# Kernel optimization log

Measured on AMD Instinct MI355X. Metric: run time of the kernel, lower is better.

Reference implementation:

```python
import jax, jax.numpy as jnp
import numpy as np

B, S, D_IN, D_OUT = 4, 2048, 4096, 11008


def setup_inputs() -> dict:
    key = jax.random.key(0)
    kx, kw, ks, kb = jax.random.split(key, 4)
    x = jax.random.normal(kx, (B, S, D_IN), dtype=jnp.float32)
    # Simulate fp8 storage: values are exactly representable in float8_e4m3fn.
    w_raw = jax.random.normal(kw, (D_OUT, D_IN), dtype=jnp.float32)
    w_q = w_raw.astype(jnp.float8_e4m3fn).astype(jnp.float32)
    # Per-output-channel dequant scale (positive).
    scale = jax.random.uniform(ks, (D_OUT, 1), dtype=jnp.float32, minval=0.01, maxval=0.1)
    bias = jax.random.normal(kb, (D_OUT,), dtype=jnp.float32)
    return {"x": x, "w_q": w_q, "scale": scale, "bias": bias}


def reference(x, w_q, scale, bias):
    # dequantize_tensor: fp8 payload * per-channel scale -> full-precision weight [D_OUT, D_IN]
    w = w_q * scale
    # F.linear(x, w, bias) = x @ w.T + bias
    out = jnp.einsum('bsd,od->bso', x, w) + bias
    return out
```

## Files before the change

kernel.cpp:

```cpp
#include <hip/hip_runtime.h>
#include <hip/hip_bf16.h>
#include <stdint.h>

#define M_DIM 8192
#define N_DIM 11008
#define K_DIM 4096
#define BM 256
#define BN 256
#define BK 32
#define NT (K_DIM / BK)
#define NBX (N_DIM / BN)
#define NBY (M_DIM / BM)
#define NBLK (NBX * NBY)
#define CPX (NBLK / 8)

typedef __bf16 bf16_8 __attribute__((ext_vector_type(8)));
typedef float f32x4 __attribute__((ext_vector_type(4)));

__device__ __forceinline__ uint32_t pack_bf2(float lo, float hi) {
    uint32_t ulo = __float_as_uint(lo);
    uint32_t uhi = __float_as_uint(hi);
    ulo = (ulo + 0x7fffu + ((ulo >> 16) & 1u)) >> 16;
    uhi = (uhi + 0x7fffu + ((uhi >> 16) & 1u)) >> 16;
    return ulo | (uhi << 16);
}

__global__ __launch_bounds__(256) void cvt_f32_bf16(const float* __restrict__ src,
                                                    uint2* __restrict__ dst, int n4) {
    int i = blockIdx.x * 256 + threadIdx.x;
    if (i >= n4) return;
    float4 a = ((const float4*)src)[i];
    uint2 o;
    o.x = pack_bf2(a.x, a.y);
    o.y = pack_bf2(a.z, a.w);
    dst[i] = o;
}

__device__ __forceinline__ void load_lds16(const __bf16* g, __bf16* l) {
    __builtin_amdgcn_global_load_lds(
        (__attribute__((address_space(1))) void*)(g),
        (__attribute__((address_space(3))) void*)(l),
        16, 0, 0);
}

#define VMCNT(n) asm volatile("s_waitcnt vmcnt(" #n ")" ::: "memory")
#define CFENCE asm volatile("" ::: "memory")

__device__ __forceinline__ void wg_barrier() {
    CFENCE;
    __builtin_amdgcn_s_barrier();
    CFENCE;
}

__device__ __forceinline__ void stage_tile(const __bf16* Ag, const __bf16* Wg,
                                           __bf16* Asl, __bf16* Bsl,
                                           int wave, long ko) {
    __bf16* la = Asl + wave * 16 * BK;
    __bf16* lb = Bsl + wave * 16 * BK;
    load_lds16(Ag + ko, la);
    load_lds16(Ag + 128 * (long)K_DIM + ko, la + 128 * BK);
    load_lds16(Wg + ko, lb);
    load_lds16(Wg + 128 * (long)K_DIM + ko, lb + 128 * BK);
}

__device__ __forceinline__ void compute_step(const __bf16* __restrict__ Abase,
                                             const __bf16* __restrict__ Bbase,
                                             f32x4 (&acc)[8][4]) {
    bf16_8 af[8], bv[4];
#pragma unroll
    for (int i = 0; i < 8; i++) af[i] = *(const bf16_8*)(Abase + i * 16 * BK);
#pragma unroll
    for (int j = 0; j < 4; j++) bv[j] = *(const bf16_8*)(Bbase + j * 16 * BK);
    __builtin_amdgcn_s_setprio(1);
#pragma unroll
    for (int i = 0; i < 8; i++)
#pragma unroll
        for (int j = 0; j < 4; j++)
            acc[i][j] = __builtin_amdgcn_mfma_f32_16x16x32_bf16(af[i], bv[j], acc[i][j], 0, 0, 0);
    __builtin_amdgcn_s_setprio(0);
}

__global__ __launch_bounds__(512, 2) void gemm_bt_scaled(
    const __bf16* __restrict__ A, const __bf16* __restrict__ W,
    const float* __restrict__ scale, const float* __restrict__ bias,
    float* __restrict__ C) {
    __shared__ __align__(16) __bf16 As[4][BM * BK];
    __shared__ __align__(16) __bf16 Bs[4][BN * BK];

    const int t = threadIdx.x;
    const int wave = t >> 6;
    const int lane = t & 63;
    const int wm = wave >> 2;
    const int wn = wave & 3;

    const int bid = (int)blockIdx.x;
    const int swz = (bid & 7) * CPX + (bid >> 3);
    const int by = swz / NBX;
    const int bx = swz - by * NBX;
    const int m0 = by * BM;
    const int n0 = bx * BN;

    const int srow = lane >> 2;
    const int sch = ((lane & 3) ^ ((lane >> 3) & 3)) * 8;
    const __bf16* Ag = A + (long)(m0 + wave * 16 + srow) * K_DIM + sch;
    const __bf16* Wg = W + (long)(n0 + wave * 16 + srow) * K_DIM + sch;

    const int lrow = lane & 15;
    const int swzr = (lrow >> 1) & 3;
    const int lk = ((lane >> 4) ^ swzr) * 8;
    const int aoff = (wm * 128 + lrow) * BK + lk;
    const int boff = (wn * 64 + lrow) * BK + lk;

    f32x4 acc[8][4] = {};

    stage_tile(Ag, Wg, &As[0][0], &Bs[0][0], wave, 0);
    stage_tile(Ag, Wg, &As[1][0], &Bs[1][0], wave, (long)BK);
    stage_tile(Ag, Wg, &As[2][0], &Bs[2][0], wave, 2L * BK);
    VMCNT(8);
    wg_barrier();

    int tt = 0;
    for (; tt < NT - 3; ++tt) {
        const int sl = tt & 3;
        const int sn = (tt + 3) & 3;
        stage_tile(Ag, Wg, &As[sn][0], &Bs[sn][0], wave, (long)(tt + 3) * BK);
        compute_step(&As[sl][aoff], &Bs[sl][boff], acc);
        VMCNT(8);
        wg_barrier();
    }
    compute_step(&As[tt & 3][aoff], &Bs[tt & 3][boff], acc);
    VMCNT(4);
    wg_barrier();
    ++tt;
    compute_step(&As[tt & 3][aoff], &Bs[tt & 3][boff], acc);
    VMCNT(0);
    wg_barrier();
    ++tt;
    compute_step(&As[tt & 3][aoff], &Bs[tt & 3][boff], acc);

    const int crow4 = (lane >> 4) * 4;
    const int ccol = lane & 15;
#pragma unroll
    for (int j = 0; j < 4; j++) {
        const int n = n0 + wn * 64 + j * 16 + ccol;
        const float sc = scale[n];
        const float bi = bias[n];
#pragma unroll
        for (int i = 0; i < 8; i++) {
            const int mbase = m0 + wm * 128 + i * 16 + crow4;
#pragma unroll
            for (int r = 0; r < 4; r++) {
                C[(long)(mbase + r) * N_DIM + n] = acc[i][j][r] * sc + bi;
            }
        }
    }
}

extern "C" void kernel_launch(void* const* d_in, const int* in_sizes, int n_in,
                              void* d_out, int out_size, void* d_ws, size_t ws_size,
                              hipStream_t stream) {
    const float* x = (const float*)d_in[0];
    const float* w_q = (const float*)d_in[1];
    const float* scale = (const float*)d_in[2];
    const float* bias = (const float*)d_in[3];
    float* out = (float*)d_out;

    __bf16* x_bf = (__bf16*)d_ws;
    __bf16* w_bf = (__bf16*)((char*)d_ws + (size_t)M_DIM * K_DIM * sizeof(__bf16));

    const int n4x = (M_DIM * K_DIM) / 4;
    const int n4w = (N_DIM * K_DIM) / 4;
    cvt_f32_bf16<<<(n4x + 255) / 256, 256, 0, stream>>>(x, (uint2*)x_bf, n4x);
    cvt_f32_bf16<<<(n4w + 255) / 256, 256, 0, stream>>>(w_q, (uint2*)w_bf, n4w);

    gemm_bt_scaled<<<dim3(NBLK), 512, 0, stream>>>(x_bf, w_bf, scale, bias, out);
}
```

Baseline: 1.533 ms.

## Split each K-step into two interleaved half-phases with staggered loads and barriers

Restructures the main loop so each K-tile is processed in two halves: read half the A fragments plus B fragments, issue the A global->LDS load, barrier, run 16 MFMAs, then read the other A half, issue the W load and run the remaining 16 MFMAs. Explicit lgkmcnt waits and sched_barriers pin the instruction order so memory issue and MFMA work from different waves interleave, in a ping-pong style. The tail is rolled into a non-unrolled loop. This adds barriers per iteration, which could cost more than the overlap gains.

```diff
diff --git a/kernel.cpp b/kernel.cpp
--- a/kernel.cpp
+++ b/kernel.cpp
@@ -44,40 +44,19 @@
 }
 
 #define VMCNT(n) asm volatile("s_waitcnt vmcnt(" #n ")" ::: "memory")
-#define CFENCE asm volatile("" ::: "memory")
+#define LGKM0    asm volatile("s_waitcnt lgkmcnt(0)" ::: "memory")
+#define SCHED0   __builtin_amdgcn_sched_barrier(0)
 
 __device__ __forceinline__ void wg_barrier() {
-    CFENCE;
+    asm volatile("" ::: "memory");
     __builtin_amdgcn_s_barrier();
-    CFENCE;
-}
-
-__device__ __forceinline__ void stage_tile(const __bf16* Ag, const __bf16* Wg,
-                                           __bf16* Asl, __bf16* Bsl,
-                                           int wave, long ko) {
-    __bf16* la = Asl + wave * 16 * BK;
-    __bf16* lb = Bsl + wave * 16 * BK;
-    load_lds16(Ag + ko, la);
-    load_lds16(Ag + 128 * (long)K_DIM + ko, la + 128 * BK);
-    load_lds16(Wg + ko, lb);
-    load_lds16(Wg + 128 * (long)K_DIM + ko, lb + 128 * BK);
-}
-
-__device__ __forceinline__ void compute_step(const __bf16* __restrict__ Abase,
-                                             const __bf16* __restrict__ Bbase,
-                                             f32x4 (&acc)[8][4]) {
-    bf16_8 af[8], bv[4];
-#pragma unroll
-    for (int i = 0; i < 8; i++) af[i] = *(const bf16_8*)(Abase + i * 16 * BK);
-#pragma unroll
-    for (int j = 0; j < 4; j++) bv[j] = *(const bf16_8*)(Bbase + j * 16 * BK);
-    __builtin_amdgcn_s_setprio(1);
-#pragma unroll
-    for (int i = 0; i < 8; i++)
-#pragma unroll
-        for (int j = 0; j < 4; j++)
-            acc[i][j] = __builtin_amdgcn_mfma_f32_16x16x32_bf16(af[i], bv[j], acc[i][j], 0, 0, 0);
-    __builtin_amdgcn_s_setprio(0);
+    asm volatile("" ::: "memory");
+}
+
+__device__ __forceinline__ void stage_pair(const __bf16* G, __bf16* L, int wave, long ko) {
+    __bf16* lw = L + wave * 16 * BK;
+    load_lds16(G + ko, lw);
+    load_lds16(G + 128L * K_DIM + ko, lw + 128 * BK);
 }
 
 __global__ __launch_bounds__(512, 2) void gemm_bt_scaled(
@@ -113,9 +92,12 @@
 
     f32x4 acc[8][4] = {};
 
-    stage_tile(Ag, Wg, &As[0][0], &Bs[0][0], wave, 0);
-    stage_tile(Ag, Wg, &As[1][0], &Bs[1][0], wave, (long)BK);
-    stage_tile(Ag, Wg, &As[2][0], &Bs[2][0], wave, 2L * BK);
+    stage_pair(Ag, &As[0][0], wave, 0);
+    stage_pair(Wg, &Bs[0][0], wave, 0);
+    stage_pair(Ag, &As[1][0], wave, (long)BK);
+    stage_pair(Wg, &Bs[1][0], wave, (long)BK);
+    stage_pair(Ag, &As[2][0], wave, 2L * BK);
+    stage_pair(Wg, &Bs[2][0], wave, 2L * BK);
     VMCNT(8);
     wg_barrier();
 
@@ -123,20 +105,68 @@
     for (; tt < NT - 3; ++tt) {
         const int sl = tt & 3;
         const int sn = (tt + 3) & 3;
-        stage_tile(Ag, Wg, &As[sn][0], &Bs[sn][0], wave, (long)(tt + 3) * BK);
-        compute_step(&As[sl][aoff], &Bs[sl][boff], acc);
+        const long ko = (long)(tt + 3) * BK;
+        const __bf16* Ab = &As[sl][aoff];
+        const __bf16* Bb = &Bs[sl][boff];
+
+        bf16_8 a0[4], bv[4];
+#pragma unroll
+        for (int i = 0; i < 4; i++) a0[i] = *(const bf16_8*)(Ab + i * 16 * BK);
+#pragma unroll
+        for (int j = 0; j < 4; j++) bv[j] = *(const bf16_8*)(Bb + j * 16 * BK);
+        stage_pair(Ag, &As[sn][0], wave, ko);
+        wg_barrier();
+        LGKM0;
+        SCHED0;
+        __builtin_amdgcn_s_setprio(1);
+#pragma unroll
+        for (int i = 0; i < 4; i++)
+#pragma unroll
+            for (int j = 0; j < 4; j++)
+                acc[i][j] = __builtin_amdgcn_mfma_f32_16x16x32_bf16(a0[i], bv[j], acc[i][j], 0, 0, 0);
+        __builtin_amdgcn_s_setprio(0);
+        SCHED0;
+        wg_barrier();
+
+        bf16_8 a1[4];
+#pragma unroll
+        for (int i = 0; i < 4; i++) a1[i] = *(const bf16_8*)(Ab + (4 + i) * 16 * BK);
+        stage_pair(Wg, &Bs[sn][0], wave, ko);
+        wg_barrier();
+        LGKM0;
+        SCHED0;
+        __builtin_amdgcn_s_setprio(1);
+#pragma unroll
+        for (int i = 0; i < 4; i++)
+#pragma unroll
+            for (int j = 0; j < 4; j++)
+                acc[4 + i][j] = __builtin_amdgcn_mfma_f32_16x16x32_bf16(a1[i], bv[j], acc[4 + i][j], 0, 0, 0);
+        __builtin_amdgcn_s_setprio(0);
+        SCHED0;
         VMCNT(8);
         wg_barrier();
     }
-    compute_step(&As[tt & 3][aoff], &Bs[tt & 3][boff], acc);
-    VMCNT(4);
-    wg_barrier();
-    ++tt;
-    compute_step(&As[tt & 3][aoff], &Bs[tt & 3][boff], acc);
-    VMCNT(0);
-    wg_barrier();
-    ++tt;
-    compute_step(&As[tt & 3][aoff], &Bs[tt & 3][boff], acc);
+
+#pragma unroll 1
+    for (int e = 0; e < 3; ++e) {
+        const int sl = (tt + e) & 3;
+        const __bf16* Ab = &As[sl][aoff];
+        const __bf16* Bb = &Bs[sl][boff];
+        bf16_8 af[8], bv[4];
+#pragma unroll
+        for (int i = 0; i < 8; i++) af[i] = *(const bf16_8*)(Ab + i * 16 * BK);
+#pragma unroll
+        for (int j = 0; j < 4; j++) bv[j] = *(const bf16_8*)(Bb + j * 16 * BK);
+        __builtin_amdgcn_s_setprio(1);
+#pragma unroll
+        for (int i = 0; i < 8; i++)
+#pragma unroll
+            for (int j = 0; j < 4; j++)
+                acc[i][j] = __builtin_amdgcn_mfma_f32_16x16x32_bf16(af[i], bv[j], acc[i][j], 0, 0, 0);
+        __builtin_amdgcn_s_setprio(0);
+        if (e == 0) { VMCNT(4); wg_barrier(); }
+        else if (e == 1) { VMCNT(0); wg_barrier(); }
+    }
 
     const int crow4 = (lane >> 4) * 4;
     const int ccol = lane & 15;
```

Measured after the change: 1.441 ms. 1.06x faster.
